# Optimization experiments

Measured on AMD Instinct MI355X. Metric: run time of the kernel, lower is better.

## Reference

```python
import jax, jax.numpy as jnp
import numpy as np

N_NODES = 20000
N_EDGES = 320000
HIDDEN = 512
EDGE_DIM = 64
LN_EPS = 1e-5


def mish(x):
    return x * jnp.tanh(jax.nn.softplus(x))


def setup_inputs() -> dict:
    key = jax.random.key(0)
    ks = jax.random.split(key, 8)
    s = lambda fan_in: 1.0 / np.sqrt(fan_in)
    return {
        "x": jax.random.normal(ks[0], (N_NODES, HIDDEN), dtype=jnp.float32),
        "edge_index": jax.random.randint(ks[1], (2, N_EDGES), 0, N_NODES, dtype=jnp.int64),
        "edge_attr": jax.random.normal(ks[2], (N_EDGES, EDGE_DIM), dtype=jnp.float32),
        "W1": jax.random.normal(ks[3], (2 * HIDDEN + EDGE_DIM, HIDDEN), dtype=jnp.float32) * s(2 * HIDDEN + EDGE_DIM),
        "b1": jnp.zeros((HIDDEN,), dtype=jnp.float32),
        "W2": jax.random.normal(ks[4], (HIDDEN, HIDDEN), dtype=jnp.float32) * s(HIDDEN),
        "b2": jnp.zeros((HIDDEN,), dtype=jnp.float32),
        "W3": jax.random.normal(ks[5], (2 * HIDDEN, HIDDEN), dtype=jnp.float32) * s(2 * HIDDEN),
        "b3": jnp.zeros((HIDDEN,), dtype=jnp.float32),
        "W4": jax.random.normal(ks[6], (HIDDEN, HIDDEN), dtype=jnp.float32) * s(HIDDEN),
        "b4": jnp.zeros((HIDDEN,), dtype=jnp.float32),
        "gamma": jnp.ones((HIDDEN,), dtype=jnp.float32),
        "beta": jnp.zeros((HIDDEN,), dtype=jnp.float32),
    }


def reference(x, edge_index, edge_attr, W1, b1, W2, b2, W3, b3, W4, b4, gamma, beta):
    src, dst = edge_index[0], edge_index[1]
    # msg_mlp: Linear -> Mish -> Linear -> Mish on [E, 2H+Edim]
    edge_feat = jnp.concatenate([x[src], x[dst], edge_attr], axis=-1)  # [E, 2H+Edim]
    h = mish(edge_feat @ W1 + b1)
    messages = mish(h @ W2 + b2)  # [E, H]
    # scatter-add messages to destination nodes
    agg = jax.ops.segment_sum(messages, dst, num_segments=x.shape[0])  # [N, H]
    # update_mlp: Linear -> Mish -> Linear
    u = mish(jnp.concatenate([x, agg], axis=-1) @ W3 + b3)
    out = u @ W4 + b4  # [N, H]
    # residual + LayerNorm
    y = x + out
    mu = jnp.mean(y, axis=-1, keepdims=True)
    var = jnp.mean(jnp.square(y - mu), axis=-1, keepdims=True)
    return (y - mu) * jax.lax.rsqrt(var + LN_EPS) * gamma + beta
```

## Files before the change

### kernel.cpp

```cpp
#include <hip/hip_runtime.h>
#include <cstdint>
#include <cstddef>

#define NNODES 20000
#define NEDGES 320000
#define HID 512
#define EDIM 64
#define KFEAT (2*HID + EDIM)

typedef __bf16 bf16x8 __attribute__((ext_vector_type(8)));
typedef short short8 __attribute__((ext_vector_type(8)));
typedef float f32x4 __attribute__((ext_vector_type(4)));

#define AM_NODE 1
#define AM_DIR  2
#define EP_BF16  0
#define EP_F32   2
#define EP_BF16L 3

__device__ __forceinline__ uint16_t f2bf(float f){
  uint32_t u = __float_as_uint(f);
  u += 0x7FFFu + ((u >> 16) & 1u);
  return (uint16_t)(u >> 16);
}
__device__ __forceinline__ float bf2f(uint16_t h){
  return __uint_as_float((uint32_t)h << 16);
}
__device__ __forceinline__ float mishf(float v){
  float e = __expf(fminf(v, 18.f));
  float n = e * (e + 2.f);
  return v * __fdividef(n, n + 2.f);
}
__device__ __forceinline__ void gl_lds16(const void* g, void* l){
  __builtin_amdgcn_global_load_lds(
      (const __attribute__((address_space(1))) uint32_t*)g,
      (__attribute__((address_space(3))) uint32_t*)l, 16, 0, 0);
}

__global__ void detect_idx(const int* __restrict__ e, int* __restrict__ flag){
  int i = blockIdx.x * 256 + threadIdx.x;
  if (e[2*i + 1] != 0) atomicOr(flag, 1);
}
__global__ void norm_idx(const int* __restrict__ e, const int* __restrict__ flag,
                         int* __restrict__ s, int* __restrict__ d){
  int i = blockIdx.x * 256 + threadIdx.x;
  if (i >= NEDGES) return;
  int sv, dv;
  if (*flag){ sv = e[i];     dv = e[NEDGES + i]; }
  else      { sv = e[2*i];   dv = e[2*NEDGES + 2*i]; }
  sv = sv < 0 ? 0 : (sv > NNODES-1 ? NNODES-1 : sv);
  dv = dv < 0 ? 0 : (dv > NNODES-1 ? NNODES-1 : dv);
  s[i] = sv; d[i] = dv;
}

__global__ void hist_k(const int* __restrict__ d, int* __restrict__ cnt){
  int i = blockIdx.x * 256 + threadIdx.x;
  if (i < NEDGES) atomicAdd(&cnt[d[i]], 1);
}
__global__ __launch_bounds__(256)
void scan_k(const int* __restrict__ cnt, int* __restrict__ rp, int* __restrict__ cur){
  const int SEG = (NNODES + 255) / 256;
  const int t = threadIdx.x;
  const int lo = t * SEG;
  const int hi = (lo + SEG < NNODES) ? lo + SEG : NNODES;
  int s = 0;
  for (int i = lo; i < hi; ++i) s += cnt[i];
  __shared__ int sh[256];
  sh[t] = s; __syncthreads();
  for (int o = 1; o < 256; o <<= 1){
    int v = (t >= o) ? sh[t - o] : 0;
    __syncthreads();
    sh[t] += v;
    __syncthreads();
  }
  int pre = t ? sh[t-1] : 0;
  for (int i = lo; i < hi; ++i){
    rp[i] = pre; cur[i] = pre; pre += cnt[i];
  }
  if (t == 255) rp[NNODES] = sh[255];
}
__global__ void permute_k(const int* __restrict__ srcN, const int* __restrict__ dstN,
                          int* __restrict__ cur, int* __restrict__ srcS,
                          int* __restrict__ eidx){
  int i = blockIdx.x * 256 + threadIdx.x;
  if (i < NEDGES){
    int d = dstN[i];
    int p = atomicAdd(&cur[d], 1);
    srcS[p] = srcN[i];
    eidx[p] = i;
  }
}
__global__ void fill_dstS(const int* __restrict__ rp, int* __restrict__ dstS){
  int n = blockIdx.x;
  int lo = rp[n], hi = rp[n+1];
  for (int e = lo + threadIdx.x; e < hi; e += 64) dstS[e] = n;
}

__global__ void cast_bf16_vec(const float4* __restrict__ in, ushort4* __restrict__ out, int n4){
  int i = blockIdx.x * 256 + threadIdx.x;
  if (i < n4){
    float4 v = in[i];
    ushort4 o; o.x = f2bf(v.x); o.y = f2bf(v.y); o.z = f2bf(v.z); o.w = f2bf(v.w);
    out[i] = o;
  }
}
__global__ void transpose_cast(const float* __restrict__ W, uint16_t* __restrict__ WT, int K, int N){
  int k = blockIdx.x * 256 + threadIdx.x;
  int n = blockIdx.y;
  if (k < K) WT[(size_t)n * K + k] = f2bf(W[(size_t)k * N + n]);
}

template<int AMODE, int EPI, int KTOT>
__global__ __launch_bounds__(256, 2)
void gemm_k(const uint16_t* __restrict__ A0, const uint16_t* __restrict__ A1,
            const uint16_t* __restrict__ BT, const float* __restrict__ bias,
            uint16_t* __restrict__ Cb, float* __restrict__ Cf,
            int bstr, int m0base, int M, int crowOff)
{
  __shared__ __align__(16) char smem[32768];
  char* As = smem;
  char* Bs = smem + 16384;
  const int t = threadIdx.x;
  const int m0 = m0base + blockIdx.x * 128;
  const int n0 = blockIdx.y * 128;
  const int srow = t >> 3;
  const int c8   = t & 7;
  const int scol = ((c8 ^ (srow & 7)) << 3);
  const int ldst = srow * 128 + c8 * 16;

  const uint16_t* as0[4]; const uint16_t* as1[4];
  #pragma unroll
  for (int i = 0; i < 4; ++i){
    int gm = m0 + srow + 32*i;
    if (gm > M - 1) gm = M - 1;
    if (AMODE == AM_NODE){
      as0[i] = A0 + (size_t)gm * HID;
      as1[i] = A1 + (size_t)gm * HID;
    } else {
      as0[i] = A0 + (size_t)gm * KTOT;
      as1[i] = A0;
    }
  }
  const uint16_t* brow[4];
  #pragma unroll
  for (int i = 0; i < 4; ++i)
    brow[i] = BT + (size_t)(n0 + srow + 32*i) * bstr;

  const int lane = t & 63;
  const int wv = t >> 6;
  const int wm = (wv >> 1) * 64;
  const int wn = (wv & 1) * 64;
  const int l15 = lane & 15;
  const int lk16 = (lane >> 4) << 4;
  const int swz = (l15 & 7) << 4;

  f32x4 acc[4][4] = {};

  const int NK = KTOT / 64;
  for (int kk = 0; kk < NK; ++kk){
    const int k0 = kk * 64;
    #pragma unroll
    for (int i = 0; i < 4; ++i){
      const uint16_t* g;
      if (AMODE == AM_NODE){
        g = (k0 < HID) ? as0[i] + (k0 + scol) : as1[i] + (k0 - HID + scol);
      } else {
        g = as0[i] + (k0 + scol);
      }
      gl_lds16(g, As + i*4096 + ldst);
    }
    #pragma unroll
    for (int i = 0; i < 4; ++i)
      gl_lds16(brow[i] + (k0 + scol), Bs + i*4096 + ldst);
    __syncthreads();
    #pragma unroll
    for (int ks = 0; ks < 2; ++ks){
      bf16x8 af[4], bfr[4];
      #pragma unroll
      for (int i = 0; i < 4; ++i){
        const int ar = wm + i*16 + l15;
        af[i] = *(const bf16x8*)(As + ar*128 + ((ks*64 + lk16) ^ swz));
      }
      #pragma unroll
      for (int j = 0; j < 4; ++j){
        const int br = wn + j*16 + l15;
        bfr[j] = *(const bf16x8*)(Bs + br*128 + ((ks*64 + lk16) ^ swz));
      }
      #pragma unroll
      for (int i = 0; i < 4; ++i)
        #pragma unroll
        for (int j = 0; j < 4; ++j)
          acc[i][j] = __builtin_amdgcn_mfma_f32_16x16x32_bf16(af[i], bfr[j], acc[i][j], 0, 0, 0);
    }
    __syncthreads();
  }

  #pragma unroll
  for (int i = 0; i < 4; ++i){
    const int rb = wm + i*16 + ((lane >> 4) << 2);
    #pragma unroll
    for (int j = 0; j < 4; ++j){
      const int gcol = n0 + wn + j*16 + l15;
      const float bv = (EPI == EP_BF16L) ? 0.f : bias[gcol];
      #pragma unroll
      for (int r = 0; r < 4; ++r){
        const int grow = m0 + rb + r;
        if (grow < M){
          float v = acc[i][j][r] + bv;
          if (EPI == EP_BF16){
            Cb[(size_t)(grow - crowOff) * HID + gcol] = f2bf(mishf(v));
          } else if (EPI == EP_BF16L){
            Cb[(size_t)(grow - crowOff) * HID + gcol] = f2bf(v);
          } else {
            Cf[(size_t)grow * HID + gcol] = v;
          }
        }
      }
    }
  }
}

__global__ __launch_bounds__(256, 2)
void eh_k(const float* __restrict__ ea, const uint16_t* __restrict__ Pb,
          const uint16_t* __restrict__ Qb, const int* __restrict__ idx,
          const uint16_t* __restrict__ w1t, const float* __restrict__ b1,
          uint16_t* __restrict__ hb, int m0base, int crowOff)
{
  __shared__ __align__(16) char smem[65536];
  const int t = threadIdx.x;
  const int m0 = m0base + blockIdx.x * 64;
  const int lane = t & 63;
  const int wv = t >> 6;
  const int l15 = lane & 15;
  const int lg = lane >> 4;
  const int* srcS = idx;
  const int* dstS = idx + NEDGES;
  const int* eidx = idx + 2*NEDGES;

  int eidxr[4];
  #pragma unroll
  for (int fr = 0; fr < 4; ++fr) eidxr[fr] = eidx[m0 + fr*16 + l15];

  float b1r[8];
  #pragma unroll
  for (int fc = 0; fc < 8; ++fc) b1r[fc] = b1[wv*128 + fc*16 + l15];

  f32x4 acc[4][8] = {};

  #pragma unroll
  for (int ks = 0; ks < 2; ++ks){
    bf16x8 bF[8];
    #pragma unroll
    for (int fc = 0; fc < 8; ++fc){
      int n = wv*128 + fc*16 + l15;
      bF[fc] = *(const bf16x8*)(w1t + (size_t)n*KFEAT + 2*HID + ks*32 + lg*8);
    }
    #pragma unroll
    for (int fr = 0; fr < 4; ++fr){
      const float4* ap = (const float4*)(ea + (size_t)eidxr[fr]*EDIM + ks*32 + lg*8);
      float4 a0 = ap[0], a1 = ap[1];
      union { short8 s; bf16x8 b; } u;
      u.s[0] = (short)f2bf(a0.x); u.s[1] = (short)f2bf(a0.y);
      u.s[2] = (short)f2bf(a0.z); u.s[3] = (short)f2bf(a0.w);
      u.s[4] = (short)f2bf(a1.x); u.s[5] = (short)f2bf(a1.y);
      u.s[6] = (short)f2bf(a1.z); u.s[7] = (short)f2bf(a1.w);
      #pragma unroll
      for (int fc = 0; fc < 8; ++fc)
        acc[fr][fc] = __builtin_amdgcn_mfma_f32_16x16x32_bf16(u.b, bF[fc], acc[fr][fc], 0, 0, 0);
    }
  }

  char* Pl = smem + wv*16384;
  char* Ql = Pl + 8192;
  #pragma unroll
  for (int half = 0; half < 2; ++half){
    #pragma unroll
    for (int p = 0; p < 8; ++p){
      int r32 = p*4 + lg;
      int grow = m0 + half*32 + r32;
      int s = srcS[grow];
      int d = dstS[grow];
      *(float4*)(Pl + r32*256 + l15*16) = *(const float4*)(Pb + (size_t)s*HID + wv*128 + l15*8);
      *(float4*)(Ql + r32*256 + l15*16) = *(const float4*)(Qb + (size_t)d*HID + wv*128 + l15*8);
    }
    __syncthreads();
    #pragma unroll
    for (int frh = 0; frh < 2; ++frh){
      int fr = half*2 + frh;
      #pragma unroll
      for (int r = 0; r < 4; ++r){
        int srow32 = frh*16 + lg*4 + r;
        size_t hrow = (size_t)(m0 + half*32 + srow32 - crowOff) * HID;
        #pragma unroll
        for (int fc = 0; fc < 8; ++fc){
          int c = fc*16 + l15;
          float pv = bf2f(*(const uint16_t*)(Pl + srow32*256 + c*2));
          float qv = bf2f(*(const uint16_t*)(Ql + srow32*256 + c*2));
          float v = acc[fr][fc][r] + pv + qv + b1r[fc];
          hb[hrow + wv*128 + c] = f2bf(mishf(v));
        }
      }
    }
    __syncthreads();
  }
}

__global__ __launch_bounds__(128)
void gather_agg(const uint16_t* __restrict__ msg, const int* __restrict__ rp,
                float* __restrict__ agg, int e0, int e1){
  const int n = blockIdx.x;
  int lo = rp[n], hi = rp[n+1];
  if (lo < e0) lo = e0;
  if (hi > e1) hi = e1;
  if (lo >= hi) return;
  const int t = threadIdx.x;
  float4 a = {0.f, 0.f, 0.f, 0.f};
  for (int e = lo; e < hi; ++e){
    ushort4 m = ((const ushort4*)(msg + (size_t)(e - e0) * HID))[t];
    a.x += bf2f(m.x); a.y += bf2f(m.y); a.z += bf2f(m.z); a.w += bf2f(m.w);
  }
  float4* ap = ((float4*)(agg + (size_t)n * HID)) + t;
  float4 c = *ap;
  c.x += a.x; c.y += a.y; c.z += a.z; c.w += a.w;
  *ap = c;
}

__global__ __launch_bounds__(128)
void resid_ln(const float* __restrict__ x, const float* __restrict__ ob,
              const float* __restrict__ gamma, const float* __restrict__ beta,
              float* __restrict__ y){
  const int row = blockIdx.x;
  const int t = threadIdx.x;
  const float4 xv = ((const float4*)(x + (size_t)row * HID))[t];
  const float4 ov = ((const float4*)(ob + (size_t)row * HID))[t];
  float4 s4;
  s4.x = xv.x + ov.x; s4.y = xv.y + ov.y; s4.z = xv.z + ov.z; s4.w = xv.w + ov.w;
  float s = s4.x + s4.y + s4.z + s4.w;
  float q = s4.x*s4.x + s4.y*s4.y + s4.z*s4.z + s4.w*s4.w;
  #pragma unroll
  for (int o = 32; o; o >>= 1){
    s += __shfl_xor(s, o, 64);
    q += __shfl_xor(q, o, 64);
  }
  __shared__ float ss[2], qq[2];
  if ((t & 63) == 0){ ss[t >> 6] = s; qq[t >> 6] = q; }
  __syncthreads();
  const float S = ss[0] + ss[1], Q = qq[0] + qq[1];
  const float mu = S * (1.0f / HID);
  const float var = Q * (1.0f / HID) - mu * mu;
  const float inv = rsqrtf(var + 1e-5f);
  const float4 g = ((const float4*)gamma)[t];
  const float4 b = ((const float4*)beta)[t];
  float4 o;
  o.x = (s4.x - mu) * inv * g.x + b.x;
  o.y = (s4.y - mu) * inv * g.y + b.y;
  o.z = (s4.z - mu) * inv * g.z + b.z;
  o.w = (s4.w - mu) * inv * g.w + b.w;
  ((float4*)(y + (size_t)row * HID))[t] = o;
}

extern "C" void kernel_launch(void* const* d_in, const int* in_sizes, int n_in,
                              void* d_out, int out_size, void* d_ws, size_t ws_size,
                              hipStream_t stream)
{
  const float* x    = (const float*)d_in[0];
  const int*   ei   = (const int*)d_in[1];
  const float* ea   = (const float*)d_in[2];
  const float* W1   = (const float*)d_in[3];
  const float* b1   = (const float*)d_in[4];
  const float* W2   = (const float*)d_in[5];
  const float* b2   = (const float*)d_in[6];
  const float* W3   = (const float*)d_in[7];
  const float* b3   = (const float*)d_in[8];
  const float* W4   = (const float*)d_in[9];
  const float* b4   = (const float*)d_in[10];
  const float* gmm  = (const float*)d_in[11];
  const float* bet  = (const float*)d_in[12];
  float* out = (float*)d_out;

  uint8_t* w = (uint8_t*)d_ws;
  size_t off = 0;
  auto alloc = [&](size_t bytes) -> void* {
    void* p = w + off;
    off += (bytes + 255) & ~(size_t)255;
    return p;
  };
  uint16_t* xb   = (uint16_t*)alloc((size_t)NNODES*HID*2);
  uint16_t* w1t  = (uint16_t*)alloc((size_t)HID*KFEAT*2);
  uint16_t* w2t  = (uint16_t*)alloc((size_t)HID*HID*2);
  uint16_t* w3t  = (uint16_t*)alloc((size_t)HID*1024*2);
  uint16_t* w4t  = (uint16_t*)alloc((size_t)HID*HID*2);
  uint16_t* Pb   = (uint16_t*)alloc((size_t)NNODES*HID*2);
  uint16_t* Qb   = (uint16_t*)alloc((size_t)NNODES*HID*2);
  float*    agg  = (float*)alloc((size_t)NNODES*HID*4);
  uint16_t* aggb = (uint16_t*)alloc((size_t)NNODES*HID*2);
  uint16_t* ub   = (uint16_t*)alloc((size_t)NNODES*HID*2);
  float*    outf = (float*)alloc((size_t)NNODES*HID*4);
  int*      srcN = (int*)alloc((size_t)NEDGES*4);
  int*      dstN = (int*)alloc((size_t)NEDGES*4);
  int*      idxS = (int*)alloc((size_t)NEDGES*4*3);
  int*      cnt  = (int*)alloc((size_t)NNODES*4);
  int*      rp   = (int*)alloc((size_t)(NNODES+1)*4);
  int*      cur  = (int*)alloc((size_t)NNODES*4);
  int*      flag = (int*)alloc(256);
  int*      srcS = idxS;
  int*      dstS = idxS + NEDGES;
  int*      eidx = idxS + 2*NEDGES;

  size_t remain = (ws_size > off) ? ws_size - off : 0;
  size_t maxChunk = remain / ((size_t)HID*2*2);
  long long chunkE = (long long)(maxChunk & ~(size_t)127);
  if (chunkE > NEDGES) chunkE = NEDGES;
  if (chunkE < 128) chunkE = 128;
  uint16_t* hb   = (uint16_t*)alloc((size_t)chunkE*HID*2);
  uint16_t* msgb = (uint16_t*)alloc((size_t)chunkE*HID*2);

  hipMemsetAsync(agg, 0, (size_t)NNODES*HID*4, stream);
  hipMemsetAsync(cnt, 0, (size_t)NNODES*4, stream);
  hipMemsetAsync(flag, 0, 4, stream);

  detect_idx<<<64, 256, 0, stream>>>(ei, flag);
  norm_idx<<<(NEDGES+255)/256, 256, 0, stream>>>(ei, flag, srcN, dstN);
  hist_k<<<(NEDGES+255)/256, 256, 0, stream>>>(dstN, cnt);
  scan_k<<<1, 256, 0, stream>>>(cnt, rp, cur);
  permute_k<<<(NEDGES+255)/256, 256, 0, stream>>>(srcN, dstN, cur, srcS, eidx);
  fill_dstS<<<NNODES, 64, 0, stream>>>(rp, dstS);

  cast_bf16_vec<<<(NNODES*HID/4+255)/256, 256, 0, stream>>>((const float4*)x, (ushort4*)xb, NNODES*HID/4);

  transpose_cast<<<dim3((KFEAT+255)/256, HID), 256, 0, stream>>>(W1, w1t, KFEAT, HID);
  transpose_cast<<<dim3((HID+255)/256,   HID), 256, 0, stream>>>(W2, w2t, HID, HID);
  transpose_cast<<<dim3((1024+255)/256,  HID), 256, 0, stream>>>(W3, w3t, 1024, HID);
  transpose_cast<<<dim3((HID+255)/256,   HID), 256, 0, stream>>>(W4, w4t, HID, HID);

  dim3 gpq((NNODES+127)/128, HID/128);
  gemm_k<AM_DIR, EP_BF16L, HID><<<gpq, 256, 0, stream>>>(
      xb, nullptr, w1t,       b1, Pb, nullptr, KFEAT, 0, NNODES, 0);
  gemm_k<AM_DIR, EP_BF16L, HID><<<gpq, 256, 0, stream>>>(
      xb, nullptr, w1t + HID, b1, Qb, nullptr, KFEAT, 0, NNODES, 0);

  for (long long e0 = 0; e0 < NEDGES; e0 += chunkE){
    int ce = (int)((NEDGES - e0 < chunkE) ? (NEDGES - e0) : chunkE);
    eh_k<<<ce/64, 256, 0, stream>>>(ea, Pb, Qb, idxS, w1t, b1, hb, (int)e0, (int)e0);
    dim3 g2((ce+127)/128, HID/128);
    gemm_k<AM_DIR, EP_BF16, HID><<<g2, 256, 0, stream>>>(
        hb, nullptr, w2t, b2, msgb, nullptr, HID, 0, ce, 0);
    gather_agg<<<NNODES, 128, 0, stream>>>(msgb, rp, agg, (int)e0, (int)(e0+ce));
  }

  cast_bf16_vec<<<(NNODES*HID/4+255)/256, 256, 0, stream>>>((const float4*)agg, (ushort4*)aggb, NNODES*HID/4);

  dim3 g3((NNODES+127)/128, HID/128);
  gemm_k<AM_NODE, EP_BF16, 1024><<<g3, 256, 0, stream>>>(
      xb, aggb, w3t, b3, ub, nullptr, 1024, 0, NNODES, 0);
  gemm_k<AM_DIR, EP_F32, HID><<<g3, 256, 0, stream>>>(
      ub, nullptr, w4t, b4, nullptr, outf, HID, 0, NNODES, 0);

  resid_ln<<<NNODES, 128, 0, stream>>>(x, outf, gmm, bet, out);
}
```

Baseline: 1.066 ms.

## Shrink edge-hidden tile to 32 rows and vectorize epilogue via per-wave LDS transpose

The edge-attribute MFMA kernel now processes 32 edges per block instead of 64, halving accumulators and shared memory, and raises the launch-bounds occupancy hint from 2 to 4. The epilogue stages the MFMA accumulators through a per-wave XOR-swizzled LDS slab so each lane reads contiguous float4 columns. This allows vectorized ushort4 loads of the P/Q rows and vectorized stores of h, and removes the block-wide __syncthreads. The trade-off is twice as many blocks, each reloading the W1 edge slice, plus an extra LDS round trip.

```diff
diff --git a/kernel.cpp b/kernel.cpp
--- a/kernel.cpp
+++ b/kernel.cpp
@@ -220,15 +220,15 @@
   }
 }
 
-__global__ __launch_bounds__(256, 2)
+__global__ __launch_bounds__(256, 4)
 void eh_k(const float* __restrict__ ea, const uint16_t* __restrict__ Pb,
           const uint16_t* __restrict__ Qb, const int* __restrict__ idx,
           const uint16_t* __restrict__ w1t, const float* __restrict__ b1,
           uint16_t* __restrict__ hb, int m0base, int crowOff)
 {
-  __shared__ __align__(16) char smem[65536];
+  __shared__ __align__(16) char smem[32768];
   const int t = threadIdx.x;
-  const int m0 = m0base + blockIdx.x * 64;
+  const int m0 = m0base + blockIdx.x * 32;
   const int lane = t & 63;
   const int wv = t >> 6;
   const int l15 = lane & 15;
@@ -237,15 +237,11 @@
   const int* dstS = idx + NEDGES;
   const int* eidx = idx + 2*NEDGES;
 
-  int eidxr[4];
-  #pragma unroll
-  for (int fr = 0; fr < 4; ++fr) eidxr[fr] = eidx[m0 + fr*16 + l15];
-
-  float b1r[8];
-  #pragma unroll
-  for (int fc = 0; fc < 8; ++fc) b1r[fc] = b1[wv*128 + fc*16 + l15];
-
-  f32x4 acc[4][8] = {};
+  int eidxr[2];
+  #pragma unroll
+  for (int fr = 0; fr < 2; ++fr) eidxr[fr] = eidx[m0 + fr*16 + l15];
+
+  f32x4 acc[2][8] = {};
 
   #pragma unroll
   for (int ks = 0; ks < 2; ++ks){
@@ -256,7 +252,7 @@
       bF[fc] = *(const bf16x8*)(w1t + (size_t)n*KFEAT + 2*HID + ks*32 + lg*8);
     }
     #pragma unroll
-    for (int fr = 0; fr < 4; ++fr){
+    for (int fr = 0; fr < 2; ++fr){
       const float4* ap = (const float4*)(ea + (size_t)eidxr[fr]*EDIM + ks*32 + lg*8);
       float4 a0 = ap[0], a1 = ap[1];
       union { short8 s; bf16x8 b; } u;
@@ -270,38 +266,49 @@
     }
   }
 
-  char* Pl = smem + wv*16384;
-  char* Ql = Pl + 8192;
-  #pragma unroll
-  for (int half = 0; half < 2; ++half){
-    #pragma unroll
-    for (int p = 0; p < 8; ++p){
-      int r32 = p*4 + lg;
-      int grow = m0 + half*32 + r32;
+  char* slab = smem + wv*8192;
+  const float4 b1v0 = *(const float4*)(b1 + wv*128 + l15*4);
+  const float4 b1v1 = *(const float4*)(b1 + wv*128 + 64 + l15*4);
+  #pragma unroll
+  for (int fr = 0; fr < 2; ++fr){
+    #pragma unroll
+    for (int fc = 0; fc < 8; ++fc){
+      #pragma unroll
+      for (int r = 0; r < 4; ++r){
+        int row = lg*4 + r;
+        int cb = ((fc*16 + l15)*4) ^ ((lg & 1) << 6);
+        *(float*)(slab + row*512 + cb) = acc[fr][fc][r];
+      }
+    }
+    asm volatile("s_waitcnt lgkmcnt(0)" ::: "memory");
+    __builtin_amdgcn_sched_barrier(0);
+    #pragma unroll
+    for (int i = 0; i < 4; ++i){
+      int row = i*4 + lg;
+      int grow = m0 + fr*16 + row;
       int s = srcS[grow];
       int d = dstS[grow];
-      *(float4*)(Pl + r32*256 + l15*16) = *(const float4*)(Pb + (size_t)s*HID + wv*128 + l15*8);
-      *(float4*)(Ql + r32*256 + l15*16) = *(const float4*)(Qb + (size_t)d*HID + wv*128 + l15*8);
-    }
-    __syncthreads();
-    #pragma unroll
-    for (int frh = 0; frh < 2; ++frh){
-      int fr = half*2 + frh;
-      #pragma unroll
-      for (int r = 0; r < 4; ++r){
-        int srow32 = frh*16 + lg*4 + r;
-        size_t hrow = (size_t)(m0 + half*32 + srow32 - crowOff) * HID;
-        #pragma unroll
-        for (int fc = 0; fc < 8; ++fc){
-          int c = fc*16 + l15;
-          float pv = bf2f(*(const uint16_t*)(Pl + srow32*256 + c*2));
-          float qv = bf2f(*(const uint16_t*)(Ql + srow32*256 + c*2));
-          float v = acc[fr][fc][r] + pv + qv + b1r[fc];
-          hb[hrow + wv*128 + c] = f2bf(mishf(v));
-        }
-      }
-    }
-    __syncthreads();
+      float4 v0 = *(const float4*)(slab + row*512 + ((l15*16) ^ ((i & 1) << 6)));
+      float4 v1 = *(const float4*)(slab + row*512 + ((256 + l15*16) ^ ((i & 1) << 6)));
+      ushort4 p0 = *(const ushort4*)(Pb + (size_t)s*HID + wv*128 + l15*4);
+      ushort4 p1 = *(const ushort4*)(Pb + (size_t)s*HID + wv*128 + 64 + l15*4);
+      ushort4 q0 = *(const ushort4*)(Qb + (size_t)d*HID + wv*128 + l15*4);
+      ushort4 q1 = *(const ushort4*)(Qb + (size_t)d*HID + wv*128 + 64 + l15*4);
+      ushort4 h0, h1;
+      h0.x = f2bf(mishf(v0.x + bf2f(p0.x) + bf2f(q0.x) + b1v0.x));
+      h0.y = f2bf(mishf(v0.y + bf2f(p0.y) + bf2f(q0.y) + b1v0.y));
+      h0.z = f2bf(mishf(v0.z + bf2f(p0.z) + bf2f(q0.z) + b1v0.z));
+      h0.w = f2bf(mishf(v0.w + bf2f(p0.w) + bf2f(q0.w) + b1v0.w));
+      h1.x = f2bf(mishf(v1.x + bf2f(p1.x) + bf2f(q1.x) + b1v1.x));
+      h1.y = f2bf(mishf(v1.y + bf2f(p1.y) + bf2f(q1.y) + b1v1.y));
+      h1.z = f2bf(mishf(v1.z + bf2f(p1.z) + bf2f(q1.z) + b1v1.z));
+      h1.w = f2bf(mishf(v1.w + bf2f(p1.w) + bf2f(q1.w) + b1v1.w));
+      size_t hrow = (size_t)(grow - crowOff) * HID + wv*128;
+      *(ushort4*)(hb + hrow + l15*4) = h0;
+      *(ushort4*)(hb + hrow + 64 + l15*4) = h1;
+    }
+    asm volatile("s_waitcnt lgkmcnt(0)" ::: "memory");
+    __builtin_amdgcn_sched_barrier(0);
   }
 }
 
@@ -441,7 +448,7 @@
 
   for (long long e0 = 0; e0 < NEDGES; e0 += chunkE){
     int ce = (int)((NEDGES - e0 < chunkE) ? (NEDGES - e0) : chunkE);
-    eh_k<<<ce/64, 256, 0, stream>>>(ea, Pb, Qb, idxS, w1t, b1, hb, (int)e0, (int)e0);
+    eh_k<<<ce/32, 256, 0, stream>>>(ea, Pb, Qb, idxS, w1t, b1, hb, (int)e0, (int)e0);
     dim3 g2((ce+127)/128, HID/128);
     gemm_k<AM_DIR, EP_BF16, HID><<<g2, 256, 0, stream>>>(
         hb, nullptr, w2t, b2, msgb, nullptr, HID, 0, ce, 0);
```

Result: faster. 980.8 us (-8.0%).

## Fuse edge hidden computation and second message GEMM into one kernel

Applied to the files above, without the earlier changes.

Merges the edge-feature layer-1 kernel and the W2 GEMM into a single kernel that keeps the 64x512 hidden tile in swizzled LDS, then runs the second MFMA GEMM straight from LDS and writes only messages. This removes the hb intermediate round-trip to global memory and one launch per chunk, and lets the chunk size double. In exchange, each block streams all of W2 from global/L2 with no tiling reuse across blocks beyond cache, and P/Q gathers become row-wise loads per wave.

```diff
diff --git a/kernel.cpp b/kernel.cpp
--- a/kernel.cpp
+++ b/kernel.cpp
@@ -10,6 +10,7 @@
 
 typedef __bf16 bf16x8 __attribute__((ext_vector_type(8)));
 typedef short short8 __attribute__((ext_vector_type(8)));
+typedef unsigned short u16x8 __attribute__((ext_vector_type(8)));
 typedef float f32x4 __attribute__((ext_vector_type(4)));
 
 #define AM_NODE 1
@@ -221,14 +222,15 @@
 }
 
 __global__ __launch_bounds__(256, 2)
-void eh_k(const float* __restrict__ ea, const uint16_t* __restrict__ Pb,
-          const uint16_t* __restrict__ Qb, const int* __restrict__ idx,
-          const uint16_t* __restrict__ w1t, const float* __restrict__ b1,
-          uint16_t* __restrict__ hb, int m0base, int crowOff)
+void edge_fuse(const float* __restrict__ ea, const uint16_t* __restrict__ Pb,
+               const uint16_t* __restrict__ Qb, const int* __restrict__ idx,
+               const uint16_t* __restrict__ w1t, const float* __restrict__ b1,
+               const uint16_t* __restrict__ w2t, const float* __restrict__ b2,
+               uint16_t* __restrict__ msgb, int e0)
 {
-  __shared__ __align__(16) char smem[65536];
+  __shared__ __align__(16) char hl[65536];
   const int t = threadIdx.x;
-  const int m0 = m0base + blockIdx.x * 64;
+  const int m0 = e0 + blockIdx.x * 64;
   const int lane = t & 63;
   const int wv = t >> 6;
   const int l15 = lane & 15;
@@ -237,16 +239,11 @@
   const int* dstS = idx + NEDGES;
   const int* eidx = idx + 2*NEDGES;
 
+  f32x4 acc[4][8] = {};
+
   int eidxr[4];
   #pragma unroll
   for (int fr = 0; fr < 4; ++fr) eidxr[fr] = eidx[m0 + fr*16 + l15];
-
-  float b1r[8];
-  #pragma unroll
-  for (int fc = 0; fc < 8; ++fc) b1r[fc] = b1[wv*128 + fc*16 + l15];
-
-  f32x4 acc[4][8] = {};
-
   #pragma unroll
   for (int ks = 0; ks < 2; ++ks){
     bf16x8 bF[8];
@@ -270,38 +267,89 @@
     }
   }
 
-  char* Pl = smem + wv*16384;
-  char* Ql = Pl + 8192;
-  #pragma unroll
-  for (int half = 0; half < 2; ++half){
-    #pragma unroll
-    for (int p = 0; p < 8; ++p){
-      int r32 = p*4 + lg;
-      int grow = m0 + half*32 + r32;
-      int s = srcS[grow];
-      int d = dstS[grow];
-      *(float4*)(Pl + r32*256 + l15*16) = *(const float4*)(Pb + (size_t)s*HID + wv*128 + l15*8);
-      *(float4*)(Ql + r32*256 + l15*16) = *(const float4*)(Qb + (size_t)d*HID + wv*128 + l15*8);
-    }
-    __syncthreads();
-    #pragma unroll
-    for (int frh = 0; frh < 2; ++frh){
-      int fr = half*2 + frh;
+  #pragma unroll
+  for (int fr = 0; fr < 4; ++fr)
+    #pragma unroll
+    for (int fc = 0; fc < 8; ++fc)
       #pragma unroll
       for (int r = 0; r < 4; ++r){
-        int srow32 = frh*16 + lg*4 + r;
-        size_t hrow = (size_t)(m0 + half*32 + srow32 - crowOff) * HID;
-        #pragma unroll
-        for (int fc = 0; fc < 8; ++fc){
-          int c = fc*16 + l15;
-          float pv = bf2f(*(const uint16_t*)(Pl + srow32*256 + c*2));
-          float qv = bf2f(*(const uint16_t*)(Ql + srow32*256 + c*2));
-          float v = acc[fr][fc][r] + pv + qv + b1r[fc];
-          hb[hrow + wv*128 + c] = f2bf(mishf(v));
-        }
+        int row = fr*16 + lg*4 + r;
+        int col = wv*128 + fc*16 + l15;
+        *(uint16_t*)(hl + row*1024 + ((col*2) ^ ((row & 7) << 4))) = f2bf(acc[fr][fc][r]);
       }
-    }
-    __syncthreads();
+  __syncthreads();
+
+  #pragma unroll 4
+  for (int rr = 0; rr < 16; ++rr){
+    int row = wv*16 + rr;
+    int grow = m0 + row;
+    int s = srcS[grow];
+    int d = dstS[grow];
+    int cb = (lane*16) ^ ((row & 7) << 4);
+    int ce = lane*8;
+    char* hp = hl + row*1024 + cb;
+    u16x8 hv = *(const u16x8*)hp;
+    u16x8 pv = *(const u16x8*)(Pb + (size_t)s*HID + ce);
+    u16x8 qv = *(const u16x8*)(Qb + (size_t)d*HID + ce);
+    const float* b1p = b1 + ce;
+    u16x8 ov;
+    #pragma unroll
+    for (int j = 0; j < 8; ++j){
+      float v = bf2f((uint16_t)hv[j]) + bf2f((uint16_t)pv[j]) + bf2f((uint16_t)qv[j]) + b1p[j];
+      ov[j] = f2bf(mishf(v));
+    }
+    *(u16x8*)hp = ov;
+  }
+  __syncthreads();
+
+  #pragma unroll
+  for (int i = 0; i < 4; ++i)
+    #pragma unroll
+    for (int j = 0; j < 8; ++j)
+      acc[i][j] = (f32x4){0.f, 0.f, 0.f, 0.f};
+  #pragma unroll 2
+  for (int ks = 0; ks < 16; ++ks){
+    bf16x8 bF[8];
+    #pragma unroll
+    for (int fc = 0; fc < 8; ++fc){
+      int n = wv*128 + fc*16 + l15;
+      bF[fc] = *(const bf16x8*)(w2t + (size_t)n*HID + ks*32 + lg*8);
+    }
+    bf16x8 af[4];
+    #pragma unroll
+    for (int i = 0; i < 4; ++i){
+      int row = i*16 + l15;
+      af[i] = *(const bf16x8*)(hl + row*1024 + ((ks*64 + lg*16) ^ ((row & 7) << 4)));
+    }
+    #pragma unroll
+    for (int i = 0; i < 4; ++i)
+      #pragma unroll
+      for (int fc = 0; fc < 8; ++fc)
+        acc[i][fc] = __builtin_amdgcn_mfma_f32_16x16x32_bf16(af[i], bF[fc], acc[i][fc], 0, 0, 0);
+  }
+  __syncthreads();
+
+  float b2r[8];
+  #pragma unroll
+  for (int fc = 0; fc < 8; ++fc) b2r[fc] = b2[wv*128 + fc*16 + l15];
+  #pragma unroll
+  for (int i = 0; i < 4; ++i)
+    #pragma unroll
+    for (int fc = 0; fc < 8; ++fc)
+      #pragma unroll
+      for (int r = 0; r < 4; ++r){
+        int row = i*16 + lg*4 + r;
+        int col = wv*128 + fc*16 + l15;
+        *(uint16_t*)(hl + row*1024 + ((col*2) ^ ((row & 7) << 4))) =
+            f2bf(mishf(acc[i][fc][r] + b2r[fc]));
+      }
+  __syncthreads();
+  #pragma unroll 4
+  for (int rr = 0; rr < 16; ++rr){
+    int row = wv*16 + rr;
+    int cb = (lane*16) ^ ((row & 7) << 4);
+    u16x8 mv = *(const u16x8*)(hl + row*1024 + cb);
+    *(u16x8*)(msgb + (size_t)(m0 - e0 + row)*HID + lane*8) = mv;
   }
 }
 
@@ -408,11 +456,10 @@
   int*      eidx = idxS + 2*NEDGES;
 
   size_t remain = (ws_size > off) ? ws_size - off : 0;
-  size_t maxChunk = remain / ((size_t)HID*2*2);
+  size_t maxChunk = remain / ((size_t)HID*2);
   long long chunkE = (long long)(maxChunk & ~(size_t)127);
   if (chunkE > NEDGES) chunkE = NEDGES;
   if (chunkE < 128) chunkE = 128;
-  uint16_t* hb   = (uint16_t*)alloc((size_t)chunkE*HID*2);
   uint16_t* msgb = (uint16_t*)alloc((size_t)chunkE*HID*2);
 
   hipMemsetAsync(agg, 0, (size_t)NNODES*HID*4, stream);
@@ -441,10 +488,8 @@
 
   for (long long e0 = 0; e0 < NEDGES; e0 += chunkE){
     int ce = (int)((NEDGES - e0 < chunkE) ? (NEDGES - e0) : chunkE);
-    eh_k<<<ce/64, 256, 0, stream>>>(ea, Pb, Qb, idxS, w1t, b1, hb, (int)e0, (int)e0);
-    dim3 g2((ce+127)/128, HID/128);
-    gemm_k<AM_DIR, EP_BF16, HID><<<g2, 256, 0, stream>>>(
-        hb, nullptr, w2t, b2, msgb, nullptr, HID, 0, ce, 0);
+    edge_fuse<<<ce/64, 256, 0, stream>>>(
+        ea, Pb, Qb, idxS, w1t, b1, w2t, b2, msgb, (int)e0);
     gather_agg<<<NNODES, 128, 0, stream>>>(msgb, rp, agg, (int)e0, (int)(e0+ce));
   }
 
```

Result: slower. 1.136 ms (+6.6%).
